# Optimization experiments

Measured on AMD Instinct MI355X. Metric: run time of the kernel, lower is better.

The kernel has to match this reference:

```python
import jax, jax.numpy as jnp
import numpy as np

B, NQ, NP = 4, 8192, 2048
DIM_INP, DIM, HID, OUT, NBLK = 256, 200, 128, 3, 5
VAR = 0.2 ** 2


def setup_inputs() -> dict:
    key = jax.random.key(0)
    ks = jax.random.split(key, 12)
    s = 0.05  # weight scale to keep activations sane
    return {
        "xyz_q": jax.random.uniform(ks[0], (B, NQ, 3), jnp.float32),
        "anchors": jax.random.uniform(ks[1], (B, NP, 3), jnp.float32),
        "anchor_feats": jax.random.normal(ks[2], (B, NP, DIM_INP), jnp.float32),
        "fc0_w": jax.random.normal(ks[3], (DIM_INP, DIM), jnp.float32) * s,
        "fc0_b": jnp.zeros((DIM,), jnp.float32),
        "fc1_w": jax.random.normal(ks[4], (DIM, HID), jnp.float32) * s,
        "fc1_b": jnp.zeros((HID,), jnp.float32),
        "blk_w0": jax.random.normal(ks[5], (NBLK, HID, HID), jnp.float32) * s,
        "blk_b0": jnp.zeros((NBLK, HID), jnp.float32),
        "blk_w1": jax.random.normal(ks[6], (NBLK, HID, HID), jnp.float32) * s,
        "blk_b1": jnp.zeros((NBLK, HID), jnp.float32),
        "fcc_w": jax.random.normal(ks[7], (NBLK, DIM, HID), jnp.float32) * s,
        "fcc_b": jnp.zeros((NBLK, HID), jnp.float32),
        "out_w": jax.random.normal(ks[8], (HID, OUT), jnp.float32) * s,
        "out_b": jnp.zeros((OUT,), jnp.float32),
    }


def reference(xyz_q, anchors, anchor_feats, fc0_w, fc0_b, fc1_w, fc1_b,
              blk_w0, blk_b0, blk_w1, blk_b1, fcc_w, fcc_b, out_w, out_b):
    relu = jax.nn.relu
    # Gaussian-kernel interpolation of anchor features at query points.
    # diff: [B, nq, np, 3]
    diff = anchors[:, None, :, :] - xyz_q[:, :, None, :]
    d = jnp.linalg.norm(diff, axis=-1)                    # [B, nq, np]
    logits = -((d + 1e-5) ** 2) / VAR
    weight = jax.nn.softmax(logits, axis=2)               # exp / sum, stable
    c = jnp.einsum('bqp,bpd->bqd', weight, anchor_feats)  # [B, nq, dim_inp]
    lat = c @ fc0_w + fc0_b                               # [B, nq, dim]
    net = relu(lat) @ fc1_w + fc1_b                       # [B, nq, hid]
    for i in range(NBLK):
        net = net + lat @ fcc_w[i] + fcc_b[i]
        # ResnetBlockFC: x + fc_1(relu(fc_0(relu(x))))
        dx = relu(relu(net) @ blk_w0[i] + blk_b0[i]) @ blk_w1[i] + blk_b1[i]
        net = net + dx
    return relu(net) @ out_w + out_b                      # [B, nq, 3]
```

## Files before the change

### kernel.cpp

```cpp
#include <hip/hip_runtime.h>
#include <math.h>

#define NP     2048
#define NQTOT  8192
#define DIN    256
#define DIM    200
#define HID    128
#define NOUT3  3
#define NBLK   5
#define TQ     32
#define NTHR   256
#define INVVAR 25.0f
#define NKT    (NP / 32)
#define NDT    16
#define NDT2   14
#define LATK   224
#define WSCALE 32768.0f
#define NFRAG  768

using f16x8 = __attribute__((ext_vector_type(8))) _Float16;
using f16x4 = __attribute__((ext_vector_type(4))) _Float16;
using f32x4 = __attribute__((ext_vector_type(4))) float;

__device__ __forceinline__ unsigned int pkrtz_u32(float a, float b) {
  auto p = __builtin_amdgcn_cvt_pkrtz(a, b);
  return __builtin_bit_cast(unsigned int, p);
}
__device__ __forceinline__ void pack_f16_2(const float* f, f16x8& h, f16x8& l) {
#pragma unroll
  for (int j = 0; j < 8; ++j) {
    const float v = f[j];
    const _Float16 hh = (_Float16)v;
    h[j] = hh; l[j] = (_Float16)(v - (float)hh);
  }
}
__device__ __forceinline__ void pack_w16(const float* f, f16x8& h, f16x8& l) {
#pragma unroll
  for (int j = 0; j < 8; ++j) {
    const float v = f[j] * WSCALE;
    const _Float16 hh = (_Float16)v;
    h[j] = hh; l[j] = (_Float16)(v - (float)hh);
  }
}
__device__ __forceinline__ void pack_a(const float* f, f16x8& h, f16x8& l) {
  union { f16x8 v; unsigned int u[4]; } H, L;
#pragma unroll
  for (int jp = 0; jp < 4; ++jp) {
    const float a = f[2 * jp], b = f[2 * jp + 1];
    auto hp = __builtin_amdgcn_cvt_pkrtz(a, b);
    H.u[jp] = __builtin_bit_cast(unsigned int, hp);
    L.u[jp] = pkrtz_u32(a - (float)hp[0], b - (float)hp[1]);
  }
  h = H.v; l = L.v;
}
__device__ __forceinline__ unsigned int split_pack(float x) {
  auto hp = __builtin_amdgcn_cvt_pkrtz(x, x);
  return pkrtz_u32(x, x - (float)hp[0]);
}

__device__ __forceinline__ int qsw(int r, int q) {
  return r * TQ + (q ^ (((r >> 2) & 7) << 2));
}
template<int KPAD>
__device__ __forceinline__ int sidx(int q, int k) {
  return q * KPAD + (((k >> 2) ^ (q & 7)) << 2) + (k & 3);
}
template<int KPAD, bool RELU>
__device__ __forceinline__ void store_split4(unsigned int* dst, int k, int qbase, f32x4 v) {
#pragma unroll
  for (int r = 0; r < 4; ++r) {
    float x = v[r];
    if (RELU) x = fmaxf(x, 0.f);
    dst[sidx<KPAD>(qbase + r, k)] = split_pack(x);
  }
}

__global__ __launch_bounds__(NTHR) void pid_packw(
    const float* __restrict__ fc0_w, const float* __restrict__ fc1_w,
    const float* __restrict__ fcc_w, const float* __restrict__ blk_w0,
    const float* __restrict__ blk_w1,
    f16x8* __restrict__ Wh, f16x8* __restrict__ Wm) {
  const int wid = threadIdx.x >> 6, l = threadIdx.x & 63;
  const int f = blockIdx.x * 4 + wid;
  if (f >= NFRAG) return;
  const float* src; int Kl, Nl, ks, nt;
  if (f < 56)       { int r = f;       src = fc1_w; Kl = 200; Nl = 128; ks = r / 8; nt = r % 8; }
  else if (f < 336) { int r = f - 56;  int i = r / 56; r %= 56;
                      src = fcc_w + (size_t)i * DIM * HID; Kl = 200; Nl = 128; ks = r / 8; nt = r % 8; }
  else if (f < 496) { int r = f - 336; int i = r / 32; r %= 32;
                      src = blk_w0 + (size_t)i * HID * HID; Kl = 128; Nl = 128; ks = r / 8; nt = r % 8; }
  else if (f < 656) { int r = f - 496; int i = r / 32; r %= 32;
                      src = blk_w1 + (size_t)i * HID * HID; Kl = 128; Nl = 128; ks = r / 8; nt = r % 8; }
  else              { int r = f - 656; src = fc0_w; Kl = 256; Nl = 200; ks = r / 14; nt = r % 14; }
  const int grp = l >> 4, n = nt * 16 + (l & 15);
  f16x8 h, m;
#pragma unroll
  for (int j = 0; j < 8; ++j) {
    const int k = ks * 32 + grp * 8 + j;
    const float v = (k < Kl && n < Nl) ? src[(size_t)k * Nl + n] : 0.f;
    const _Float16 hh = (_Float16)v;
    h[j] = hh; m[j] = (_Float16)(v - (float)hh);
  }
  const size_t fi = (size_t)f * 64 + l;
  Wh[fi] = h; Wm[fi] = m;
}

__global__ __launch_bounds__(NTHR) void pid_packfw(
    const float* __restrict__ F,
    const f16x8* __restrict__ Wh, const f16x8* __restrict__ Wm,
    _Float16* __restrict__ outH, _Float16* __restrict__ outL) {
  const int t = threadIdx.x;
  const int w = t >> 6, l = t & 63;
  const int grp = l >> 4, qn = l & 15;
  const int pt = blockIdx.x * 2 + (w >> 1);
  const int nh = w & 1;
  const int batch = pt >> 7, ptl = pt & 127;
  const int kt = ptl >> 1;
  const int grp2 = ((ptl & 1) << 1) + (grp >> 1);

  f32x4 acc[7];
#pragma unroll
  for (int j = 0; j < 7; ++j) acc[j] = (f32x4){0.f, 0.f, 0.f, 0.f};

  const float* fa0 = F + ((size_t)batch * NP + ptl * 16 + qn) * DIN + grp * 8;
#pragma unroll 1
  for (int ks = 0; ks < 8; ++ks) {
    float av8[8];
    *(float4*)&av8[0] = *(const float4*)(fa0 + ks * 32);
    *(float4*)&av8[4] = *(const float4*)(fa0 + ks * 32 + 4);
    f16x8 ah, al;
    pack_f16_2(av8, ah, al);
#pragma unroll
    for (int nt2 = 0; nt2 < 7; ++nt2) {
      const size_t fi = (size_t)(656 + ks * 14 + nh * 7 + nt2) * 64 + l;
      const f16x8 bh = Wh[fi], bm = Wm[fi];
      f32x4 a = acc[nt2];
      a = __builtin_amdgcn_mfma_f32_16x16x32_f16(ah, bh, a, 0, 0, 0);
      a = __builtin_amdgcn_mfma_f32_16x16x32_f16(ah, bm, a, 0, 0, 0);
      a = __builtin_amdgcn_mfma_f32_16x16x32_f16(al, bh, a, 0, 0, 0);
      acc[nt2] = a;
    }
  }
#pragma unroll
  for (int nt2 = 0; nt2 < 7; ++nt2) {
    const int nt = nh * 7 + nt2;
    f16x4 hv, lv;
#pragma unroll
    for (int r = 0; r < 4; ++r) {
      const float v = acc[nt2][r];
      const _Float16 hh = (_Float16)v;
      hv[r] = hh; lv[r] = (_Float16)(v - (float)hh);
    }
    const size_t base =
        (((size_t)(batch * 64 + kt) * NDT2 + nt) * 64 + grp2 * 16 + qn) * 8 +
        (grp & 1) * 4;
    *(f16x4*)(outH + base) = hv;
    *(f16x4*)(outL + base) = lv;
  }
}

__global__ __launch_bounds__(NTHR) void pid_packf16(const float* __restrict__ F,
                                                    f16x8* __restrict__ wsHi,
                                                    f16x8* __restrict__ wsLo) {
  const int wid = threadIdx.x >> 6, l = threadIdx.x & 63;
  const int tile = blockIdx.x * 4 + wid;
  const int b  = tile >> 10;
  const int kt = (tile >> 4) & 63;
  const int dt = tile & 15;
  const int grp = l >> 4, qn = l & 15;
  const float* src = F + ((size_t)b * NP + kt * 32 + grp * 8) * DIN + dt * 16 + qn;
  float v[8];
#pragma unroll
  for (int j = 0; j < 8; ++j) v[j] = src[(size_t)j * DIN];
  f16x8 h, lo;
  pack_f16_2(v, h, lo);
  const size_t fi = (size_t)tile * 64 + l;
  wsHi[fi] = h; wsLo[fi] = lo;
}

template<int KS, int NT, int MAXNT, int KPADIN, bool RELUA>
__device__ __forceinline__ void mm_stage(
    const unsigned int* __restrict__ Xs,
    const f16x8* __restrict__ Wh, const f16x8* __restrict__ Wm, int fbase,
    f32x4 acc[2][MAXNT], int wid, int l) {
  const int grp = l >> 4, qn = l & 15;
  f16x8 bhA[MAXNT], bmA[MAXNT], bhB[MAXNT], bmB[MAXNT];

#define LOADF(BH, BM, KSV)                                                    \
  _Pragma("unroll") for (int i = 0; i < MAXNT; ++i) {                         \
    const int nt = wid + i * 4;                                               \
    if (nt < NT) {                                                            \
      const size_t fi = (size_t)(fbase + (KSV) * NT + nt) * 64 + l;           \
      BH[i] = Wh[fi]; BM[i] = Wm[fi];                                         \
    }                                                                         \
  }

#define COMPUTE(KSV, BH, BM)                                                  \
  {                                                                           \
    const int u0 = (KSV) * 8 + grp * 2;                                       \
    f16x8 ah[2], al[2];                                                       \
    _Pragma("unroll") for (int qt = 0; qt < 2; ++qt) {                        \
      const int q = qt * 16 + qn;                                             \
      const unsigned int* row = Xs + q * KPADIN;                              \
      const uint4 lo = *(const uint4*)(row + (((u0) ^ (q & 7)) << 2));        \
      const uint4 hi = *(const uint4*)(row + (((u0 + 1) ^ (q & 7)) << 2));    \
      unsigned int p[8] = {lo.x, lo.y, lo.z, lo.w, hi.x, hi.y, hi.z, hi.w};   \
      if (RELUA) {                                                            \
        _Pragma("unroll") for (int j = 0; j < 8; ++j)                         \
          p[j] = (p[j] & 0x8000u) ? 0u : p[j];                                \
      }                                                                       \
      union { f16x8 v; unsigned int u[4]; } H, L;                             \
      _Pragma("unroll") for (int jp = 0; jp < 4; ++jp) {                      \
        H.u[jp] = __builtin_amdgcn_perm(p[2 * jp + 1], p[2 * jp], 0x05040100u);\
        L.u[jp] = __builtin_amdgcn_perm(p[2 * jp + 1], p[2 * jp], 0x07060302u);\
      }                                                                       \
      ah[qt] = H.v; al[qt] = L.v;                                             \
    }                                                                         \
    _Pragma("unroll") for (int qt = 0; qt < 2; ++qt)                          \
    _Pragma("unroll") for (int i = 0; i < MAXNT; ++i)                         \
      if (wid + i * 4 < NT) {                                                 \
        acc[qt][i] = __builtin_amdgcn_mfma_f32_16x16x32_f16(ah[qt], BH[i], acc[qt][i], 0, 0, 0); \
        acc[qt][i] = __builtin_amdgcn_mfma_f32_16x16x32_f16(ah[qt], BM[i], acc[qt][i], 0, 0, 0); \
        acc[qt][i] = __builtin_amdgcn_mfma_f32_16x16x32_f16(al[qt], BH[i], acc[qt][i], 0, 0, 0); \
      }                                                                       \
  }

  LOADF(bhA, bmA, 0)
#pragma unroll 1
  for (int ks = 0; ks + 1 < KS; ks += 2) {
    LOADF(bhB, bmB, ks + 1)
    COMPUTE(ks, bhA, bmA)
    if (ks + 2 < KS) { LOADF(bhA, bmA, ks + 2) }
    COMPUTE(ks + 1, bhB, bmB)
  }
  if (KS & 1) { COMPUTE(KS - 1, bhA, bmA) }
#undef LOADF
#undef COMPUTE
}

struct SMemV2 {
  union {
    struct { float ax[NP * 3]; float qx[TQ], qy[TQ], qz[TQ]; } a;
    unsigned int lats[32 * LATK];
  } r1;
  union {
    float4 exch[28 * 64];
    struct { unsigned int nets[32 * 128]; unsigned int tmps[32 * 128]; } nt;
    float netf[128 * 32];
  } r2;
  float sS[64];
};

__global__ __launch_bounds__(NTHR, 2) void pid_fused_mfma(
    const float* __restrict__ xyz_q, const float* __restrict__ anchors,
    const f16x8* __restrict__ wsFh, const f16x8* __restrict__ wsFl,
    const f16x8* __restrict__ Wh, const f16x8* __restrict__ Wm,
    const float* __restrict__ fc0_b, const float* __restrict__ fc1_b,
    const float* __restrict__ blk_b0, const float* __restrict__ blk_b1,
    const float* __restrict__ fcc_b,
    const float* __restrict__ out_w, const float* __restrict__ out_b,
    float* __restrict__ out) {
  __shared__ SMemV2 sm;
  const int t = threadIdx.x;
  const int bi = blockIdx.x;
  const int batch = bi & 3;
  const int q0 = (bi >> 2) * TQ;

  {
    const float4* src = (const float4*)(anchors + (size_t)batch * NP * 3);
    float4* dst = (float4*)sm.r1.a.ax;
#pragma unroll
    for (int j = 0; j < (NP * 3 / 4) / NTHR; ++j)
      dst[j * NTHR + t] = src[j * NTHR + t];
  }
  if (t < TQ) {
    const float* qp = xyz_q + ((size_t)batch * NQTOT + q0 + t) * 3;
    sm.r1.a.qx[t] = qp[0]; sm.r1.a.qy[t] = qp[1]; sm.r1.a.qz[t] = qp[2];
  }
  __syncthreads();

  const int wid = t >> 6, l = t & 63;
  const int kp = wid & 1;
  const int dh = wid >> 1;
  const int grp = l >> 4, qn = l & 15;
  const float q0x = sm.r1.a.qx[qn],      q0y = sm.r1.a.qy[qn],      q0z = sm.r1.a.qz[qn];
  const float q1x = sm.r1.a.qx[16 + qn], q1y = sm.r1.a.qy[16 + qn], q1z = sm.r1.a.qz[16 + qn];
  const float nC1 = -36.067376f;
  const float nC2 = -7.2134752e-4f;

  const f16x8* pH = wsFh + ((size_t)(batch * 64 + kp) * NDT2 + dh * 7) * 64 + l;
  const f16x8* pL = wsFl + ((size_t)(batch * 64 + kp) * NDT2 + dh * 7) * 64 + l;

  f32x4 acc[2][7];
#pragma unroll
  for (int a = 0; a < 2; ++a)
#pragma unroll
    for (int j = 0; j < 7; ++j) acc[a][j] = (f32x4){0.f, 0.f, 0.f, 0.f};
  float s0 = 0.f, s1 = 0.f;

#pragma unroll 1
  for (int kt = kp; kt < NKT; kt += 2) {
    f16x8 bh[7], bl[7];
#pragma unroll
    for (int k = 0; k < 7; ++k) { bh[k] = pH[k * 64]; bl[k] = pL[k * 64]; }

    const int pb = kt * 32 + grp * 8;
    float4 av[6];
    {
      const float4* ap = (const float4*)&sm.r1.a.ax[pb * 3];
#pragma unroll
      for (int j = 0; j < 6; ++j) av[j] = ap[j];
    }
    const float* af = (const float*)av;
    float w8[8];
#pragma unroll
    for (int j = 0; j < 8; ++j) {
      const float dx = af[3 * j] - q0x, dy = af[3 * j + 1] - q0y, dz = af[3 * j + 2] - q0z;
      const float D = fmaf(dx, dx, fmaf(dy, dy, dz * dz));
      const float s = __builtin_amdgcn_sqrtf(D);
      const float u = __builtin_amdgcn_exp2f(fmaf(nC2, s, fmaf(nC1, D, 15.0f)));
      w8[j] = u; s0 += u;
    }
    f16x8 ah0, al0;
    pack_a(w8, ah0, al0);
#pragma unroll
    for (int j = 0; j < 8; ++j) {
      const float dx = af[3 * j] - q1x, dy = af[3 * j + 1] - q1y, dz = af[3 * j + 2] - q1z;
      const float D = fmaf(dx, dx, fmaf(dy, dy, dz * dz));
      const float s = __builtin_amdgcn_sqrtf(D);
      const float u = __builtin_amdgcn_exp2f(fmaf(nC2, s, fmaf(nC1, D, 15.0f)));
      w8[j] = u; s1 += u;
    }
    f16x8 ah1, al1;
    pack_a(w8, ah1, al1);

#define MM3(ACC, AH, AL, BH, BL)                                              \
    ACC = __builtin_amdgcn_mfma_f32_16x16x32_f16(AH, BH, ACC, 0, 0, 0);       \
    ACC = __builtin_amdgcn_mfma_f32_16x16x32_f16(AH, BL, ACC, 0, 0, 0);       \
    ACC = __builtin_amdgcn_mfma_f32_16x16x32_f16(AL, BH, ACC, 0, 0, 0);
#pragma unroll
    for (int k = 0; k < 7; ++k) {
      MM3(acc[0][k], ah0, al0, bh[k], bl[k])
      MM3(acc[1][k], ah1, al1, bh[k], bl[k])
    }
#undef MM3
    pH += 2 * NDT2 * 64; pL += 2 * NDT2 * 64;
  }

  s0 += __shfl_xor(s0, 16); s0 += __shfl_xor(s0, 32);
  s1 += __shfl_xor(s1, 16); s1 += __shfl_xor(s1, 32);
  if (dh == 0 && l < 16) {
    sm.sS[kp * 32 + qn] = s0;
    sm.sS[kp * 32 + 16 + qn] = s1;
  }
  float4* P = sm.r2.exch;
  if (kp == 0) {
#pragma unroll
    for (int qt2 = 0; qt2 < 2; ++qt2)
#pragma unroll
      for (int d2 = 0; d2 < 7; ++d2)
        P[(qt2 * 14 + dh * 7 + d2) * 64 + grp * 16 + qn] =
            make_float4(acc[qt2][d2][0], acc[qt2][d2][1],
                        acc[qt2][d2][2], acc[qt2][d2][3]);
  }
  __syncthreads();
  if (kp == 1) {
    float sc0[4], sc1[4];
#pragma unroll
    for (int r = 0; r < 4; ++r) {
      const int j = grp * 4 + r;
      sc0[r] = __builtin_amdgcn_rcpf(sm.sS[j] + sm.sS[32 + j]);
      sc1[r] = __builtin_amdgcn_rcpf(sm.sS[16 + j] + sm.sS[48 + j]);
    }
#pragma unroll
    for (int d2 = 0; d2 < 7; ++d2) {
      const int k = (dh * 7 + d2) * 16 + qn;
      const float bb = (k < DIM) ? fc0_b[k] : 0.f;
      const float4 p0 = P[(0 * 14 + dh * 7 + d2) * 64 + grp * 16 + qn];
      const float4 p1 = P[(1 * 14 + dh * 7 + d2) * 64 + grp * 16 + qn];
      const f32x4 v0 = {fmaf(acc[0][d2][0] + p0.x, sc0[0], bb),
                        fmaf(acc[0][d2][1] + p0.y, sc0[1], bb),
                        fmaf(acc[0][d2][2] + p0.z, sc0[2], bb),
                        fmaf(acc[0][d2][3] + p0.w, sc0[3], bb)};
      store_split4<LATK, false>(sm.r1.lats, k, grp * 4, v0);
      const f32x4 v1 = {fmaf(acc[1][d2][0] + p1.x, sc1[0], bb),
                        fmaf(acc[1][d2][1] + p1.y, sc1[1], bb),
                        fmaf(acc[1][d2][2] + p1.z, sc1[2], bb),
                        fmaf(acc[1][d2][3] + p1.w, sc1[3], bb)};
      store_split4<LATK, false>(sm.r1.lats, k, 16 + grp * 4, v1);
    }
  }
  __syncthreads();

  f32x4 net[2][2];
#pragma unroll
  for (int i = 0; i < 2; ++i) {
    const float b = fc1_b[(wid + i * 4) * 16 + qn];
#pragma unroll
    for (int q2 = 0; q2 < 2; ++q2) net[q2][i] = (f32x4){b, b, b, b};
  }
  mm_stage<7, 8, 2, LATK, true>(sm.r1.lats, Wh, Wm, 0, net, wid, l);

#pragma unroll 1
  for (int ib = 0; ib < NBLK; ++ib) {
#pragma unroll
    for (int i = 0; i < 2; ++i) {
      const float b = fcc_b[ib * HID + (wid + i * 4) * 16 + qn];
#pragma unroll
      for (int q2 = 0; q2 < 2; ++q2) net[q2][i] += (f32x4){b, b, b, b};
    }
    mm_stage<7, 8, 2, LATK, false>(sm.r1.lats, Wh, Wm, 56 + 56 * ib, net, wid, l);
#pragma unroll
    for (int q2 = 0; q2 < 2; ++q2)
#pragma unroll
      for (int i = 0; i < 2; ++i)
        store_split4<128, true>(sm.r2.nt.nets, (wid + i * 4) * 16 + qn,
                                q2 * 16 + grp * 4, net[q2][i]);
    __syncthreads();
    f32x4 a2[2][2];
#pragma unroll
    for (int i = 0; i < 2; ++i) {
      const float b = blk_b0[ib * HID + (wid + i * 4) * 16 + qn];
#pragma unroll
      for (int q2 = 0; q2 < 2; ++q2) a2[q2][i] = (f32x4){b, b, b, b};
    }
    mm_stage<4, 8, 2, 128, false>(sm.r2.nt.nets, Wh, Wm, 336 + 32 * ib, a2, wid, l);
#pragma unroll
    for (int q2 = 0; q2 < 2; ++q2)
#pragma unroll
      for (int i = 0; i < 2; ++i)
        store_split4<128, true>(sm.r2.nt.tmps, (wid + i * 4) * 16 + qn,
                                q2 * 16 + grp * 4, a2[q2][i]);
    __syncthreads();
#pragma unroll
    for (int i = 0; i < 2; ++i) {
      const float b = blk_b1[ib * HID + (wid + i * 4) * 16 + qn];
#pragma unroll
      for (int q2 = 0; q2 < 2; ++q2) net[q2][i] += (f32x4){b, b, b, b};
    }
    mm_stage<4, 8, 2, 128, false>(sm.r2.nt.tmps, Wh, Wm, 496 + 32 * ib, net, wid, l);
  }
  __syncthreads();

#pragma unroll
  for (int q2 = 0; q2 < 2; ++q2)
#pragma unroll
    for (int i = 0; i < 2; ++i) {
      const int n = (wid + i * 4) * 16 + qn;
      *(float4*)&sm.r2.netf[n * 32 + q2 * 16 + grp * 4] =
          make_float4(net[q2][i][0], net[q2][i][1], net[q2][i][2], net[q2][i][3]);
    }
  __syncthreads();
  if (t < TQ * NOUT3) {
    const int q = t / NOUT3, n = t - q * NOUT3;
    float s = out_b[n];
#pragma unroll 8
    for (int k = 0; k < HID; ++k)
      s = fmaf(fmaxf(sm.r2.netf[k * 32 + q], 0.f), out_w[k * NOUT3 + n], s);
    out[((size_t)batch * NQTOT + q0 + q) * NOUT3 + n] = s;
  }
}

template<int K, bool RELUX, bool ACCY>
__device__ __forceinline__ void stage_h128(const float* __restrict__ X,
                                           const float* __restrict__ Wg,
                                           const float* __restrict__ bg,
                                           float* __restrict__ Y, int t) {
  const int qg = t & 7, ng = t >> 3;
  const int n0 = ng * 4, q0 = qg * 4;
  const float4 bv = *(const float4*)&bg[n0];
  const float br[4] = {bv.x, bv.y, bv.z, bv.w};
  float acc[4][4];
#pragma unroll
  for (int j = 0; j < 4; ++j) {
    if (ACCY) {
      const float4 yv = *(const float4*)&Y[qsw(n0 + j, q0)];
      acc[0][j] = yv.x + br[j]; acc[1][j] = yv.y + br[j];
      acc[2][j] = yv.z + br[j]; acc[3][j] = yv.w + br[j];
    } else {
      acc[0][j] = br[j]; acc[1][j] = br[j]; acc[2][j] = br[j]; acc[3][j] = br[j];
    }
  }
#pragma unroll 2
  for (int k0 = 0; k0 < K; k0 += 8) {
    float4 wr[8];
#pragma unroll
    for (int kk = 0; kk < 8; ++kk)
      wr[kk] = *(const float4*)&Wg[(size_t)(k0 + kk) * HID + n0];
#pragma unroll
    for (int kk = 0; kk < 8; ++kk) {
      float4 xv = *(const float4*)&X[qsw(k0 + kk, q0)];
      if (RELUX) {
        xv.x = fmaxf(xv.x, 0.f); xv.y = fmaxf(xv.y, 0.f);
        xv.z = fmaxf(xv.z, 0.f); xv.w = fmaxf(xv.w, 0.f);
      }
      const float xr[4] = {xv.x, xv.y, xv.z, xv.w};
      const float wl[4] = {wr[kk].x, wr[kk].y, wr[kk].z, wr[kk].w};
#pragma unroll
      for (int i = 0; i < 4; ++i)
#pragma unroll
        for (int j = 0; j < 4; ++j)
          acc[i][j] = fmaf(xr[i], wl[j], acc[i][j]);
    }
  }
#pragma unroll
  for (int j = 0; j < 4; ++j)
    *(float4*)&Y[qsw(n0 + j, q0)] =
        make_float4(acc[0][j], acc[1][j], acc[2][j], acc[3][j]);
}

__device__ __forceinline__ void stage_fc0v(const float* __restrict__ X,
                                           const float* __restrict__ Wg,
                                           const float* __restrict__ bg,
                                           float* __restrict__ Y, int t) {
  const int qg = t & 7, ng = t >> 3;
  const int n0 = ng * 8, q0 = qg * 4;
  const bool act = (ng < 25);
  float acc[4][8];
  if (act) {
    const float4 b0 = *(const float4*)&bg[n0];
    const float4 b1 = *(const float4*)&bg[n0 + 4];
    const float br[8] = {b0.x, b0.y, b0.z, b0.w, b1.x, b1.y, b1.z, b1.w};
#pragma unroll
    for (int j = 0; j < 8; ++j)
#pragma unroll
      for (int i = 0; i < 4; ++i) acc[i][j] = br[j];
  }
#pragma unroll 2
  for (int k0 = 0; k0 < DIN; k0 += 4) {
    if (act) {
      float4 wa[4], wb[4];
#pragma unroll
      for (int kk = 0; kk < 4; ++kk) {
        wa[kk] = *(const float4*)&Wg[(size_t)(k0 + kk) * DIM + n0];
        wb[kk] = *(const float4*)&Wg[(size_t)(k0 + kk) * DIM + n0 + 4];
      }
#pragma unroll
      for (int kk = 0; kk < 4; ++kk) {
        const float4 xv = *(const float4*)&X[qsw(k0 + kk, q0)];
        const float xr[4] = {xv.x, xv.y, xv.z, xv.w};
        const float wl[8] = {wa[kk].x, wa[kk].y, wa[kk].z, wa[kk].w,
                             wb[kk].x, wb[kk].y, wb[kk].z, wb[kk].w};
#pragma unroll
        for (int i = 0; i < 4; ++i)
#pragma unroll
          for (int j = 0; j < 8; ++j)
            acc[i][j] = fmaf(xr[i], wl[j], acc[i][j]);
      }
    }
  }
  if (act) {
#pragma unroll
    for (int j = 0; j < 8; ++j)
      *(float4*)&Y[qsw(n0 + j, q0)] =
          make_float4(acc[0][j], acc[1][j], acc[2][j], acc[3][j]);
  }
}

struct SA1 {
  float ax[NP * 3];
  float qx[TQ], qy[TQ], qz[TQ], m[TQ];
  float sred[8 * TQ];
};
struct SB1 {
  float lat[DIM * TQ];
  union {
    float cT[DIN * TQ];
    struct { float net[HID * TQ]; float tmp[HID * TQ]; } nt;
  } u;
};
struct SMem1 { union { SA1 a; SB1 b; } s; float sS[TQ]; };

__global__ __launch_bounds__(NTHR, 2) void pid_fused_vec(
    const float* __restrict__ xyz_q, const float* __restrict__ anchors,
    const f16x8* __restrict__ wsFh, const f16x8* __restrict__ wsFl,
    const float* __restrict__ fc0_w, const float* __restrict__ fc0_b,
    const float* __restrict__ fc1_w, const float* __restrict__ fc1_b,
    const float* __restrict__ blk_w0, const float* __restrict__ blk_b0,
    const float* __restrict__ blk_w1, const float* __restrict__ blk_b1,
    const float* __restrict__ fcc_w, const float* __restrict__ fcc_b,
    const float* __restrict__ out_w, const float* __restrict__ out_b,
    float* __restrict__ out) {
  __shared__ SMem1 sm;
  const int t = threadIdx.x;
  const int bi = blockIdx.x;
  const int batch = bi & 3;
  const int q0 = (bi >> 2) * TQ;

  {
    const float4* src = (const float4*)(anchors + (size_t)batch * NP * 3);
    float4* dst = (float4*)sm.s.a.ax;
#pragma unroll
    for (int j = 0; j < (NP * 3 / 4) / NTHR; ++j)
      dst[j * NTHR + t] = src[j * NTHR + t];
  }
  if (t < TQ) {
    const float* qp = xyz_q + ((size_t)batch * NQTOT + q0 + t) * 3;
    sm.s.a.qx[t] = qp[0]; sm.s.a.qy[t] = qp[1]; sm.s.a.qz[t] = qp[2];
  }
  __syncthreads();
  {
    const int q = t & 31, g = t >> 5;
    const float qxv = sm.s.a.qx[q], qyv = sm.s.a.qy[q], qzv = sm.s.a.qz[q];
    float mloc = 3.0e38f;
    const float* az = sm.s.a.ax + g * 256 * 3;
    for (int pi = 0; pi < 256; ++pi) {
      const float dx = az[pi * 3 + 0] - qxv;
      const float dy = az[pi * 3 + 1] - qyv;
      const float dz = az[pi * 3 + 2] - qzv;
      mloc = fminf(mloc, fmaf(dx, dx, fmaf(dy, dy, dz * dz)));
    }
    sm.s.a.sred[g * TQ + q] = mloc;
  }
  __syncthreads();
  if (t < TQ) {
    float mv = sm.s.a.sred[t];
#pragma unroll
    for (int g = 1; g < 8; ++g) mv = fminf(mv, sm.s.a.sred[g * TQ + t]);
    const float dmin = sqrtf(mv) + 1e-5f;
    sm.s.a.m[t] = -dmin * dmin * INVVAR;
  }
  __syncthreads();

  const int wid = t >> 6, l = t & 63;
  const int qt = wid & 1;
  const int dgb = (wid >> 1) * 8;
  const int grp = l >> 4, qn = l & 15;
  const float qxv = sm.s.a.qx[qt * 16 + qn];
  const float qyv = sm.s.a.qy[qt * 16 + qn];
  const float qzv = sm.s.a.qz[qt * 16 + qn];
  const float negm = -sm.s.a.m[qt * 16 + qn];
  const f16x8* BH = wsFh + (size_t)batch * NKT * NDT * 64;
  const f16x8* BL = wsFl + (size_t)batch * NKT * NDT * 64;

  f32x4 acc[8];
#pragma unroll
  for (int j = 0; j < 8; ++j) acc[j] = (f32x4){0.f, 0.f, 0.f, 0.f};
  float ssum = 0.f;
#pragma unroll 1
  for (int kt = 0; kt < NKT; ++kt) {
    f16x8 bh[8], bl[8];
#pragma unroll
    for (int d2 = 0; d2 < 8; ++d2) {
      const size_t fi = ((size_t)kt * NDT + dgb + d2) * 64 + l;
      bh[d2] = BH[fi]; bl[d2] = BL[fi];
    }
    const int pb = kt * 32 + grp * 8;
    float4 av[6];
    {
      const float4* ap = (const float4*)&sm.s.a.ax[pb * 3];
#pragma unroll
      for (int j = 0; j < 6; ++j) av[j] = ap[j];
    }
    const float* af = (const float*)av;
    float w8[8];
#pragma unroll
    for (int j = 0; j < 8; ++j) {
      const float dx = af[3 * j] - qxv, dy = af[3 * j + 1] - qyv, dz = af[3 * j + 2] - qzv;
      const float d = sqrtf(fmaf(dx, dx, fmaf(dy, dy, dz * dz))) + 1e-5f;
      const float u = __expf(fmaf(d * d, -INVVAR, negm));
      w8[j] = u; ssum += u;
    }
    f16x8 ah, al;
    pack_w16(w8, ah, al);
#pragma unroll
    for (int d2 = 0; d2 < 8; ++d2)
      acc[d2] = __builtin_amdgcn_mfma_f32_16x16x32_f16(ah, bh[d2], acc[d2], 0, 0, 0);
#pragma unroll
    for (int d2 = 0; d2 < 8; ++d2)
      acc[d2] = __builtin_amdgcn_mfma_f32_16x16x32_f16(ah, bl[d2], acc[d2], 0, 0, 0);
#pragma unroll
    for (int d2 = 0; d2 < 8; ++d2)
      acc[d2] = __builtin_amdgcn_mfma_f32_16x16x32_f16(al, bh[d2], acc[d2], 0, 0, 0);
  }
  ssum += __shfl_xor(ssum, 16);
  ssum += __shfl_xor(ssum, 32);
  if (wid < 2 && grp == 0) sm.sS[qt * 16 + qn] = ssum;
  __syncthreads();
  float sc[4];
#pragma unroll
  for (int r = 0; r < 4; ++r)
    sc[r] = (1.0f / WSCALE) / sm.sS[qt * 16 + grp * 4 + r];
#pragma unroll
  for (int d2 = 0; d2 < 8; ++d2) {
    const int d = (dgb + d2) * 16 + qn;
    *(float4*)&sm.s.b.u.cT[qsw(d, qt * 16 + grp * 4)] =
        make_float4(acc[d2][0] * sc[0], acc[d2][1] * sc[1],
                    acc[d2][2] * sc[2], acc[d2][3] * sc[3]);
  }
  __syncthreads();

  stage_fc0v(sm.s.b.u.cT, fc0_w, fc0_b, sm.s.b.lat, t);
  __syncthreads();
  stage_h128<DIM, true, false>(sm.s.b.lat, fc1_w, fc1_b, sm.s.b.u.nt.net, t);
  __syncthreads();
#pragma unroll 1
  for (int i = 0; i < NBLK; ++i) {
    stage_h128<DIM, false, true>(sm.s.b.lat, fcc_w + (size_t)i * DIM * HID,
                                 fcc_b + i * HID, sm.s.b.u.nt.net, t);
    __syncthreads();
    stage_h128<HID, true, false>(sm.s.b.u.nt.net, blk_w0 + (size_t)i * HID * HID,
                                 blk_b0 + i * HID, sm.s.b.u.nt.tmp, t);
    __syncthreads();
    stage_h128<HID, true, true>(sm.s.b.u.nt.tmp, blk_w1 + (size_t)i * HID * HID,
                                blk_b1 + i * HID, sm.s.b.u.nt.net, t);
    __syncthreads();
  }
  if (t < TQ * NOUT3) {
    const int q = t / NOUT3, n = t - q * NOUT3;
    float s = out_b[n];
    const float* net = sm.s.b.u.nt.net;
#pragma unroll 8
    for (int k = 0; k < HID; ++k)
      s = fmaf(fmaxf(net[k * TQ + (q ^ (((k >> 2) & 7) << 2))], 0.f),
               out_w[k * NOUT3 + n], s);
    out[((size_t)batch * NQTOT + q0 + q) * NOUT3 + n] = s;
  }
}

extern "C" void kernel_launch(void* const* d_in, const int* in_sizes, int n_in,
                              void* d_out, int out_size, void* d_ws, size_t ws_size,
                              hipStream_t stream) {
  (void)in_sizes; (void)n_in; (void)out_size;
  const float* xyz_q        = (const float*)d_in[0];
  const float* anchors      = (const float*)d_in[1];
  const float* anchor_feats = (const float*)d_in[2];
  const float* fc0_w        = (const float*)d_in[3];
  const float* fc0_b        = (const float*)d_in[4];
  const float* fc1_w        = (const float*)d_in[5];
  const float* fc1_b        = (const float*)d_in[6];
  const float* blk_w0       = (const float*)d_in[7];
  const float* blk_b0       = (const float*)d_in[8];
  const float* blk_w1       = (const float*)d_in[9];
  const float* blk_b1       = (const float*)d_in[10];
  const float* fcc_w        = (const float*)d_in[11];
  const float* fcc_b        = (const float*)d_in[12];
  const float* out_w        = (const float*)d_in[13];
  const float* out_b        = (const float*)d_in[14];
  float* out = (float*)d_out;

  const size_t F2_BYTES = (size_t)4 * 64 * NDT2 * 64 * 16;
  const size_t W2_BYTES = (size_t)NFRAG * 64 * 16;
  if (ws_size >= 2 * F2_BYTES + 2 * W2_BYTES) {
    f16x8* wsFh = (f16x8*)d_ws;
    f16x8* wsFl = (f16x8*)((char*)d_ws + F2_BYTES);
    f16x8* Wh   = (f16x8*)((char*)d_ws + 2 * F2_BYTES);
    f16x8* Wm   = (f16x8*)((char*)d_ws + 2 * F2_BYTES + W2_BYTES);
    hipLaunchKernelGGL(pid_packw, dim3((NFRAG + 3) / 4), dim3(NTHR), 0, stream,
                       fc0_w, fc1_w, fcc_w, blk_w0, blk_w1, Wh, Wm);
    hipLaunchKernelGGL(pid_packfw, dim3(256), dim3(NTHR), 0, stream,
                       anchor_feats, Wh, Wm, (_Float16*)wsFh, (_Float16*)wsFl);
    hipLaunchKernelGGL(pid_fused_mfma, dim3(1024), dim3(NTHR), 0, stream,
                       xyz_q, anchors, wsFh, wsFl, Wh, Wm,
                       fc0_b, fc1_b, blk_b0, blk_b1, fcc_b, out_w, out_b, out);
  } else {
    const size_t F1_BYTES = (size_t)4 * NKT * NDT * 64 * 16;
    f16x8* wsFh = (f16x8*)d_ws;
    f16x8* wsFl = (f16x8*)((char*)d_ws + F1_BYTES);
    hipLaunchKernelGGL(pid_packf16, dim3(1024), dim3(NTHR), 0, stream,
                       anchor_feats, wsFh, wsFl);
    hipLaunchKernelGGL(pid_fused_vec, dim3(1024), dim3(NTHR), 0, stream,
                       xyz_q, anchors, wsFh, wsFl,
                       fc0_w, fc0_b, fc1_w, fc1_b, blk_w0, blk_b0,
                       blk_w1, blk_b1, fcc_w, fcc_b, out_w, out_b, out);
  }
}
```

Baseline: 239.7 us.

## Double fused kernel block to 512 threads with 4-way K split and 8-wave MLP

The fused MFMA kernel now launches 512 threads (8 waves) per block instead of 256. The softmax-interpolation loop over anchor tiles is split four ways instead of two, with a two-level shared-memory reduction of partial accumulators and row sums. The MLP stages give each wave one 16-column output tile instead of two, halving per-wave register pressure. The intent is more waves in flight for latency hiding, at the cost of extra barriers and reduction traffic, plus a higher occupancy target in launch_bounds that may limit registers.

```diff
diff --git a/kernel.cpp b/kernel.cpp
--- a/kernel.cpp
+++ b/kernel.cpp
@@ -10,6 +10,7 @@
 #define NBLK   5
 #define TQ     32
 #define NTHR   256
+#define NTHR2  512
 #define INVVAR 25.0f
 #define NKT    (NP / 32)
 #define NDT    16
@@ -178,21 +179,18 @@
   wsHi[fi] = h; wsLo[fi] = lo;
 }
 
-template<int KS, int NT, int MAXNT, int KPADIN, bool RELUA>
-__device__ __forceinline__ void mm_stage(
+template<int KS, int KPADIN, bool RELUA>
+__device__ __forceinline__ void mm_stage8(
     const unsigned int* __restrict__ Xs,
     const f16x8* __restrict__ Wh, const f16x8* __restrict__ Wm, int fbase,
-    f32x4 acc[2][MAXNT], int wid, int l) {
+    f32x4 acc[2], int wid, int l) {
   const int grp = l >> 4, qn = l & 15;
-  f16x8 bhA[MAXNT], bmA[MAXNT], bhB[MAXNT], bmB[MAXNT];
+  f16x8 bhA, bmA, bhB, bmB;
 
 #define LOADF(BH, BM, KSV)                                                    \
-  _Pragma("unroll") for (int i = 0; i < MAXNT; ++i) {                         \
-    const int nt = wid + i * 4;                                               \
-    if (nt < NT) {                                                            \
-      const size_t fi = (size_t)(fbase + (KSV) * NT + nt) * 64 + l;           \
-      BH[i] = Wh[fi]; BM[i] = Wm[fi];                                         \
-    }                                                                         \
+  {                                                                           \
+    const size_t fi = (size_t)(fbase + (KSV) * 8 + wid) * 64 + l;             \
+    BH = Wh[fi]; BM = Wm[fi];                                                 \
   }
 
 #define COMPUTE(KSV, BH, BM)                                                  \
@@ -216,13 +214,11 @@
       }                                                                       \
       ah[qt] = H.v; al[qt] = L.v;                                             \
     }                                                                         \
-    _Pragma("unroll") for (int qt = 0; qt < 2; ++qt)                          \
-    _Pragma("unroll") for (int i = 0; i < MAXNT; ++i)                         \
-      if (wid + i * 4 < NT) {                                                 \
-        acc[qt][i] = __builtin_amdgcn_mfma_f32_16x16x32_f16(ah[qt], BH[i], acc[qt][i], 0, 0, 0); \
-        acc[qt][i] = __builtin_amdgcn_mfma_f32_16x16x32_f16(ah[qt], BM[i], acc[qt][i], 0, 0, 0); \
-        acc[qt][i] = __builtin_amdgcn_mfma_f32_16x16x32_f16(al[qt], BH[i], acc[qt][i], 0, 0, 0); \
-      }                                                                       \
+    _Pragma("unroll") for (int qt = 0; qt < 2; ++qt) {                        \
+      acc[qt] = __builtin_amdgcn_mfma_f32_16x16x32_f16(ah[qt], BH, acc[qt], 0, 0, 0); \
+      acc[qt] = __builtin_amdgcn_mfma_f32_16x16x32_f16(ah[qt], BM, acc[qt], 0, 0, 0); \
+      acc[qt] = __builtin_amdgcn_mfma_f32_16x16x32_f16(al[qt], BH, acc[qt], 0, 0, 0); \
+    }                                                                         \
   }
 
   LOADF(bhA, bmA, 0)
@@ -242,16 +238,17 @@
   union {
     struct { float ax[NP * 3]; float qx[TQ], qy[TQ], qz[TQ]; } a;
     unsigned int lats[32 * LATK];
+    float4 exq[28 * 64];
   } r1;
   union {
     float4 exch[28 * 64];
     struct { unsigned int nets[32 * 128]; unsigned int tmps[32 * 128]; } nt;
     float netf[128 * 32];
   } r2;
-  float sS[64];
+  float sS[128];
 };
 
-__global__ __launch_bounds__(NTHR, 2) void pid_fused_mfma(
+__global__ __launch_bounds__(NTHR2, 4) void pid_fused_mfma(
     const float* __restrict__ xyz_q, const float* __restrict__ anchors,
     const f16x8* __restrict__ wsFh, const f16x8* __restrict__ wsFl,
     const f16x8* __restrict__ Wh, const f16x8* __restrict__ Wm,
@@ -270,8 +267,8 @@
     const float4* src = (const float4*)(anchors + (size_t)batch * NP * 3);
     float4* dst = (float4*)sm.r1.a.ax;
 #pragma unroll
-    for (int j = 0; j < (NP * 3 / 4) / NTHR; ++j)
-      dst[j * NTHR + t] = src[j * NTHR + t];
+    for (int j = 0; j < 3; ++j)
+      dst[j * NTHR2 + t] = src[j * NTHR2 + t];
   }
   if (t < TQ) {
     const float* qp = xyz_q + ((size_t)batch * NQTOT + q0 + t) * 3;
@@ -280,8 +277,8 @@
   __syncthreads();
 
   const int wid = t >> 6, l = t & 63;
-  const int kp = wid & 1;
-  const int dh = wid >> 1;
+  const int kp = wid & 3;
+  const int dh = wid >> 2;
   const int grp = l >> 4, qn = l & 15;
   const float q0x = sm.r1.a.qx[qn],      q0y = sm.r1.a.qy[qn],      q0z = sm.r1.a.qz[qn];
   const float q1x = sm.r1.a.qx[16 + qn], q1y = sm.r1.a.qy[16 + qn], q1z = sm.r1.a.qz[16 + qn];
@@ -299,7 +296,7 @@
   float s0 = 0.f, s1 = 0.f;
 
 #pragma unroll 1
-  for (int kt = kp; kt < NKT; kt += 2) {
+  for (int kt = kp; kt < NKT; kt += 4) {
     f16x8 bh[7], bl[7];
 #pragma unroll
     for (int k = 0; k < 7; ++k) { bh[k] = pH[k * 64]; bl[k] = pL[k * 64]; }
@@ -344,7 +341,7 @@
       MM3(acc[1][k], ah1, al1, bh[k], bl[k])
     }
 #undef MM3
-    pH += 2 * NDT2 * 64; pL += 2 * NDT2 * 64;
+    pH += 4 * NDT2 * 64; pL += 4 * NDT2 * 64;
   }
 
   s0 += __shfl_xor(s0, 16); s0 += __shfl_xor(s0, 32);
@@ -353,103 +350,110 @@
     sm.sS[kp * 32 + qn] = s0;
     sm.sS[kp * 32 + 16 + qn] = s1;
   }
+  __syncthreads();
+
   float4* P = sm.r2.exch;
+  float4* Q = sm.r1.exq;
+#define WRITE_PART(BUF)                                                       \
+  _Pragma("unroll") for (int qt2 = 0; qt2 < 2; ++qt2)                         \
+  _Pragma("unroll") for (int d2 = 0; d2 < 7; ++d2)                            \
+    BUF[(qt2 * 14 + dh * 7 + d2) * 64 + grp * 16 + qn] =                      \
+        make_float4(acc[qt2][d2][0], acc[qt2][d2][1],                         \
+                    acc[qt2][d2][2], acc[qt2][d2][3]);
+#define ADD_PART(BUF)                                                         \
+  _Pragma("unroll") for (int qt2 = 0; qt2 < 2; ++qt2)                         \
+  _Pragma("unroll") for (int d2 = 0; d2 < 7; ++d2) {                          \
+    const float4 pv = BUF[(qt2 * 14 + dh * 7 + d2) * 64 + grp * 16 + qn];     \
+    acc[qt2][d2][0] += pv.x; acc[qt2][d2][1] += pv.y;                         \
+    acc[qt2][d2][2] += pv.z; acc[qt2][d2][3] += pv.w;                         \
+  }
+  if (kp == 1) { WRITE_PART(P) }
+  if (kp == 3) { WRITE_PART(Q) }
+  __syncthreads();
+  if (kp == 0) { ADD_PART(P) }
+  if (kp == 2) { ADD_PART(Q) }
+  __syncthreads();
+  if (kp == 2) { WRITE_PART(P) }
+  __syncthreads();
   if (kp == 0) {
-#pragma unroll
-    for (int qt2 = 0; qt2 < 2; ++qt2)
-#pragma unroll
-      for (int d2 = 0; d2 < 7; ++d2)
-        P[(qt2 * 14 + dh * 7 + d2) * 64 + grp * 16 + qn] =
-            make_float4(acc[qt2][d2][0], acc[qt2][d2][1],
-                        acc[qt2][d2][2], acc[qt2][d2][3]);
-  }
-  __syncthreads();
-  if (kp == 1) {
+    ADD_PART(P)
     float sc0[4], sc1[4];
 #pragma unroll
     for (int r = 0; r < 4; ++r) {
       const int j = grp * 4 + r;
-      sc0[r] = __builtin_amdgcn_rcpf(sm.sS[j] + sm.sS[32 + j]);
-      sc1[r] = __builtin_amdgcn_rcpf(sm.sS[16 + j] + sm.sS[48 + j]);
+      sc0[r] = __builtin_amdgcn_rcpf(sm.sS[j] + sm.sS[32 + j] +
+                                     sm.sS[64 + j] + sm.sS[96 + j]);
+      sc1[r] = __builtin_amdgcn_rcpf(sm.sS[16 + j] + sm.sS[48 + j] +
+                                     sm.sS[80 + j] + sm.sS[112 + j]);
     }
 #pragma unroll
     for (int d2 = 0; d2 < 7; ++d2) {
       const int k = (dh * 7 + d2) * 16 + qn;
       const float bb = (k < DIM) ? fc0_b[k] : 0.f;
-      const float4 p0 = P[(0 * 14 + dh * 7 + d2) * 64 + grp * 16 + qn];
-      const float4 p1 = P[(1 * 14 + dh * 7 + d2) * 64 + grp * 16 + qn];
-      const f32x4 v0 = {fmaf(acc[0][d2][0] + p0.x, sc0[0], bb),
-                        fmaf(acc[0][d2][1] + p0.y, sc0[1], bb),
-                        fmaf(acc[0][d2][2] + p0.z, sc0[2], bb),
-                        fmaf(acc[0][d2][3] + p0.w, sc0[3], bb)};
+      const f32x4 v0 = {fmaf(acc[0][d2][0], sc0[0], bb),
+                        fmaf(acc[0][d2][1], sc0[1], bb),
+                        fmaf(acc[0][d2][2], sc0[2], bb),
+                        fmaf(acc[0][d2][3], sc0[3], bb)};
       store_split4<LATK, false>(sm.r1.lats, k, grp * 4, v0);
-      const f32x4 v1 = {fmaf(acc[1][d2][0] + p1.x, sc1[0], bb),
-                        fmaf(acc[1][d2][1] + p1.y, sc1[1], bb),
-                        fmaf(acc[1][d2][2] + p1.z, sc1[2], bb),
-                        fmaf(acc[1][d2][3] + p1.w, sc1[3], bb)};
+      const f32x4 v1 = {fmaf(acc[1][d2][0], sc1[0], bb),
+                        fmaf(acc[1][d2][1], sc1[1], bb),
+                        fmaf(acc[1][d2][2], sc1[2], bb),
+                        fmaf(acc[1][d2][3], sc1[3], bb)};
       store_split4<LATK, false>(sm.r1.lats, k, 16 + grp * 4, v1);
     }
   }
-  __syncthreads();
-
-  f32x4 net[2][2];
-#pragma unroll
-  for (int i = 0; i < 2; ++i) {
-    const float b = fc1_b[(wid + i * 4) * 16 + qn];
-#pragma unroll
-    for (int q2 = 0; q2 < 2; ++q2) net[q2][i] = (f32x4){b, b, b, b};
-  }
-  mm_stage<7, 8, 2, LATK, true>(sm.r1.lats, Wh, Wm, 0, net, wid, l);
+#undef WRITE_PART
+#undef ADD_PART
+  __syncthreads();
+
+  f32x4 net[2];
+#pragma unroll
+  for (int q2 = 0; q2 < 2; ++q2) {
+    const float b = fc1_b[wid * 16 + qn];
+    net[q2] = (f32x4){b, b, b, b};
+  }
+  mm_stage8<7, LATK, true>(sm.r1.lats, Wh, Wm, 0, net, wid, l);
 
 #pragma unroll 1
   for (int ib = 0; ib < NBLK; ++ib) {
-#pragma unroll
-    for (int i = 0; i < 2; ++i) {
-      const float b = fcc_b[ib * HID + (wid + i * 4) * 16 + qn];
-#pragma unroll
-      for (int q2 = 0; q2 < 2; ++q2) net[q2][i] += (f32x4){b, b, b, b};
-    }
-    mm_stage<7, 8, 2, LATK, false>(sm.r1.lats, Wh, Wm, 56 + 56 * ib, net, wid, l);
+    {
+      const float b = fcc_b[ib * HID + wid * 16 + qn];
+#pragma unroll
+      for (int q2 = 0; q2 < 2; ++q2) net[q2] += (f32x4){b, b, b, b};
+    }
+    mm_stage8<7, LATK, false>(sm.r1.lats, Wh, Wm, 56 + 56 * ib, net, wid, l);
 #pragma unroll
     for (int q2 = 0; q2 < 2; ++q2)
-#pragma unroll
-      for (int i = 0; i < 2; ++i)
-        store_split4<128, true>(sm.r2.nt.nets, (wid + i * 4) * 16 + qn,
-                                q2 * 16 + grp * 4, net[q2][i]);
+      store_split4<128, true>(sm.r2.nt.nets, wid * 16 + qn,
+                              q2 * 16 + grp * 4, net[q2]);
     __syncthreads();
-    f32x4 a2[2][2];
-#pragma unroll
-    for (int i = 0; i < 2; ++i) {
-      const float b = blk_b0[ib * HID + (wid + i * 4) * 16 + qn];
-#pragma unroll
-      for (int q2 = 0; q2 < 2; ++q2) a2[q2][i] = (f32x4){b, b, b, b};
-    }
-    mm_stage<4, 8, 2, 128, false>(sm.r2.nt.nets, Wh, Wm, 336 + 32 * ib, a2, wid, l);
+    f32x4 a2[2];
+    {
+      const float b = blk_b0[ib * HID + wid * 16 + qn];
+#pragma unroll
+      for (int q2 = 0; q2 < 2; ++q2) a2[q2] = (f32x4){b, b, b, b};
+    }
+    mm_stage8<4, 128, false>(sm.r2.nt.nets, Wh, Wm, 336 + 32 * ib, a2, wid, l);
 #pragma unroll
     for (int q2 = 0; q2 < 2; ++q2)
-#pragma unroll
-      for (int i = 0; i < 2; ++i)
-        store_split4<128, true>(sm.r2.nt.tmps, (wid + i * 4) * 16 + qn,
-                                q2 * 16 + grp * 4, a2[q2][i]);
+      store_split4<128, true>(sm.r2.nt.tmps, wid * 16 + qn,
+                              q2 * 16 + grp * 4, a2[q2]);
     __syncthreads();
-#pragma unroll
-    for (int i = 0; i < 2; ++i) {
-      const float b = blk_b1[ib * HID + (wid + i * 4) * 16 + qn];
-#pragma unroll
-      for (int q2 = 0; q2 < 2; ++q2) net[q2][i] += (f32x4){b, b, b, b};
-    }
-    mm_stage<4, 8, 2, 128, false>(sm.r2.nt.tmps, Wh, Wm, 496 + 32 * ib, net, wid, l);
-  }
-  __syncthreads();
-
-#pragma unroll
-  for (int q2 = 0; q2 < 2; ++q2)
-#pragma unroll
-    for (int i = 0; i < 2; ++i) {
-      const int n = (wid + i * 4) * 16 + qn;
-      *(float4*)&sm.r2.netf[n * 32 + q2 * 16 + grp * 4] =
-          make_float4(net[q2][i][0], net[q2][i][1], net[q2][i][2], net[q2][i][3]);
-    }
+    {
+      const float b = blk_b1[ib * HID + wid * 16 + qn];
+#pragma unroll
+      for (int q2 = 0; q2 < 2; ++q2) net[q2] += (f32x4){b, b, b, b};
+    }
+    mm_stage8<4, 128, false>(sm.r2.nt.tmps, Wh, Wm, 496 + 32 * ib, net, wid, l);
+  }
+  __syncthreads();
+
+#pragma unroll
+  for (int q2 = 0; q2 < 2; ++q2) {
+    const int n = wid * 16 + qn;
+    *(float4*)&sm.r2.netf[n * 32 + q2 * 16 + grp * 4] =
+        make_float4(net[q2][0], net[q2][1], net[q2][2], net[q2][3]);
+  }
   __syncthreads();
   if (t < TQ * NOUT3) {
     const int q = t / NOUT3, n = t - q * NOUT3;
@@ -750,7 +754,7 @@
                        fc0_w, fc1_w, fcc_w, blk_w0, blk_w1, Wh, Wm);
     hipLaunchKernelGGL(pid_packfw, dim3(256), dim3(NTHR), 0, stream,
                        anchor_feats, Wh, Wm, (_Float16*)wsFh, (_Float16*)wsFl);
-    hipLaunchKernelGGL(pid_fused_mfma, dim3(1024), dim3(NTHR), 0, stream,
+    hipLaunchKernelGGL(pid_fused_mfma, dim3(1024), dim3(NTHR2), 0, stream,
                        xyz_q, anchors, wsFh, wsFl, Wh, Wm,
                        fc0_b, fc1_b, blk_b0, blk_b1, fcc_b, out_w, out_b, out);
   } else {
```

Result: slower. 289.2 us (+20.7%).
